# Optimization experiments

Measured on AMD Instinct MI355X. Metric: run time of the kernel, lower is better.

Reference implementation:

```python
import jax, jax.numpy as jnp
import numpy as np
from functools import partial

TAU = 2.0       # membrane time constant
V_TH = 1.0      # firing threshold
SLOPE = 10.0    # surrogate sigmoid slope (matches rate_encode's 10*)
T = 10          # time_window
H = 12          # num_heads


def lif_step(v, I):
    """One LIF update: leaky integrate, surrogate spike, multiplicative reset."""
    v = v + (I - v) / TAU
    spk = jax.nn.sigmoid(SLOPE * (v - V_TH))
    v = v * (1.0 - spk)
    return spk, v


def setup_inputs() -> dict:
    key = jax.random.key(0)
    ks = jax.random.split(key, 5)
    B, S, E = 8, 1024, 768
    scale = 1.0 / np.sqrt(E)
    x = jax.random.uniform(ks[0], (B, S, E), dtype=jnp.float32)
    Wq = jax.random.normal(ks[1], (E, E), dtype=jnp.float32) * scale
    Wk = jax.random.normal(ks[2], (E, E), dtype=jnp.float32) * scale
    Wv = jax.random.normal(ks[3], (E, E), dtype=jnp.float32) * scale
    Wo = jax.random.normal(ks[4], (E, E), dtype=jnp.float32) * scale
    zb = jnp.zeros((E,), dtype=jnp.float32)
    return {"x": x, "Wq": Wq, "bq": zb, "Wk": Wk, "bk": zb,
            "Wv": Wv, "bv": zb, "Wo": Wo, "bo": zb}


def reference(x, Wq, bq, Wk, bk, Wv, bv, Wo, bo):
    B, S, E = x.shape
    D = E // H
    # rate encoding probability (x assumed in [0,1] range, clipped)
    p = jnp.clip(x, 0.0, 1.0)  # [B,S,E]

    def step(carry, t):
        vq, vk, vv, Qa, Ka, Va = carry
        inp = jax.nn.sigmoid(SLOPE * (p * T - t))  # [B,S,E] spikes at step t
        qs, vq = lif_step(vq, inp @ Wq.T + bq)
        ks, vk = lif_step(vk, inp @ Wk.T + bk)
        vs, vv = lif_step(vv, inp @ Wv.T + bv)
        return (vq, vk, vv, Qa + qs, Ka + ks, Va + vs), None

    z = jnp.zeros((B, S, E), dtype=x.dtype)
    t_idx = jnp.arange(T, dtype=x.dtype)
    (vq, vk, vv, Q, K, V), _ = jax.lax.scan(step, (z, z, z, z, z, z), t_idx)

    # split heads: [B,S,E] -> [B,H,S,D]
    Qh = Q.reshape(B, S, H, D)
    Kh = K.reshape(B, S, H, D)
    Vh = V.reshape(B, S, H, D)
    scores = jnp.einsum('bqhd,bkhd->bhqk', Qh, Kh) / np.sqrt(D)
    attn = jax.nn.softmax(scores, axis=-1)
    out_h = jnp.einsum('bhqk,bkhd->bqhd', attn, Vh)  # [B,S,H,D]
    out = out_h.reshape(B, S, E)
    # output LIF projection with fresh (zero) state
    out_spk, _ = lif_step(jnp.zeros_like(out), out @ Wo.T + bo)
    return out_spk
```

## Files before the change

### kernel.cpp

```cpp
#include <hip/hip_runtime.h>
#include <math.h>

constexpr int B_ = 8, S_ = 1024, E_ = 768, H_ = 12, D_ = 64, T_ = 10;
constexpr int N_ = B_ * S_;
constexpr int NE_ = N_ * E_;
constexpr int WE_ = E_ * E_;

typedef __attribute__((ext_vector_type(8))) short bf16x8;
typedef __attribute__((ext_vector_type(4))) float f32x4;

#define MFMA16(a,b,c) __builtin_amdgcn_mfma_f32_16x16x32_bf16(a,b,c,0,0,0)

__device__ __forceinline__ float sigm(float z){ return 1.f/(1.f+__expf(-z)); }
__device__ __forceinline__ unsigned short f2bf(float f){
    unsigned int u = __float_as_uint(f);
    u += 0x7FFFu + ((u>>16)&1u);
    return (unsigned short)(u>>16);
}
__device__ __forceinline__ float bf2f(unsigned short h){
    return __uint_as_float(((unsigned int)h)<<16);
}
__device__ __forceinline__ void gl16(const void* g, void* l){
    __builtin_amdgcn_global_load_lds((const __attribute__((address_space(1))) unsigned int*)g,
                                     (__attribute__((address_space(3))) unsigned int*)l, 16, 0, 0);
}

__global__ __launch_bounds__(256) void encode_k(const float* __restrict__ x,
                                                unsigned short* __restrict__ enc){
    const int i = blockIdx.x*256 + threadIdx.x;
    const float4 a = ((const float4*)x)[2*i];
    const float4 b = ((const float4*)x)[2*i+1];
    float p[8] = {a.x,a.y,a.z,a.w,b.x,b.y,b.z,b.w};
#pragma unroll
    for (int e=0;e<8;++e) p[e] = 100.f*fminf(fmaxf(p[e],0.f),1.f);
#pragma unroll
    for (int t=0;t<T_;++t){
        unsigned int w[4];
#pragma unroll
        for (int e=0;e<4;++e){
            unsigned short u0 = f2bf(sigm(p[2*e]   - 10.f*(float)t));
            unsigned short u1 = f2bf(sigm(p[2*e+1] - 10.f*(float)t));
            w[e] = (unsigned int)u0 | ((unsigned int)u1<<16);
        }
        ((uint4*)(enc + (long)t*NE_))[i] = make_uint4(w[0],w[1],w[2],w[3]);
    }
}

__global__ __launch_bounds__(256) void wsplit_k(const float* __restrict__ Wq, const float* __restrict__ Wk,
        const float* __restrict__ Wv, const float* __restrict__ Wo,
        unsigned short* __restrict__ whi, unsigned short* __restrict__ wlo){
    int gi = blockIdx.x*256 + threadIdx.x;
    int z = gi / (WE_/8);
    int r = gi % (WE_/8);
    const float* W = z==0?Wq : z==1?Wk : z==2?Wv : Wo;
    const float4 a = ((const float4*)W)[2*r];
    const float4 b = ((const float4*)W)[2*r+1];
    float f[8]={a.x,a.y,a.z,a.w,b.x,b.y,b.z,b.w};
    unsigned int h[4], l[4];
#pragma unroll
    for (int e=0;e<4;++e){
        unsigned short h0=f2bf(f[2*e]),   l0=f2bf(f[2*e]  -bf2f(h0));
        unsigned short h1=f2bf(f[2*e+1]), l1=f2bf(f[2*e+1]-bf2f(h1));
        h[e] = (unsigned)h0 | ((unsigned)h1<<16);
        l[e] = (unsigned)l0 | ((unsigned)l1<<16);
    }
    ((uint4*)(whi + (long)z*WE_))[r] = make_uint4(h[0],h[1],h[2],h[3]);
    ((uint4*)(wlo + (long)z*WE_))[r] = make_uint4(l[0],l[1],l[2],l[3]);
}

__global__ __launch_bounds__(256,2) void qkv_k(const unsigned short* __restrict__ enc,
        const unsigned short* __restrict__ whi,
        const float* __restrict__ bq, const float* __restrict__ bk, const float* __restrict__ bv,
        float* __restrict__ Qf, float* __restrict__ Kf, float* __restrict__ Vf){
    const int z = blockIdx.z;
    const unsigned short* Wh = whi + (long)z*WE_;
    const float* bias = z==0?bq : z==1?bk : bv;
    float* Out = z==0?Qf : z==1?Kf : Vf;
    const int row0 = blockIdx.x*128, col0 = blockIdx.y*64;

    __shared__ unsigned short Ab[128*64];
    __shared__ unsigned short Bh[64*64];

    const int tid = threadIdx.x, lane = tid&63, wid = tid>>6;
    const int l15 = lane&15, l4 = lane>>4, l7 = lane&7;
    const int wr = wid>>1, wc = wid&1;

    int aSrc[4], bSrc[2];
#pragma unroll
    for (int s=0;s<4;++s){
        int idx = (wid + s*4)*64 + lane;
        int row = idx>>3, ch = idx&7;
        aSrc[s] = (row0+row)*E_ + ((ch ^ (row&7))<<3);
    }
#pragma unroll
    for (int s=0;s<2;++s){
        int idx = (wid + s*4)*64 + lane;
        int row = idx>>3, ch = idx&7;
        bSrc[s] = (col0+row)*E_ + ((ch ^ (row&7))<<3);
    }

    const int aBase = (wr*64 + l15)*128;
    const int bBase = (wc*32 + l15)*128;
    const int sw[2] = { ((l4^l7)<<4), ((((4+l4))^l7)<<4) };

    f32x4 acc[4][2];
    float vm[4][2][4] = {};
    float qa[4][2][4] = {};
    float bn[2];
#pragma unroll
    for (int n=0;n<2;++n) bn[n] = bias[col0 + wc*32 + n*16 + l15];
    const f32x4 zero4 = {0.f,0.f,0.f,0.f};

    for (int t=0;t<T_;++t){
        const long tb = (long)t*NE_;
#pragma unroll
        for (int m=0;m<4;++m)
#pragma unroll
            for (int n=0;n<2;++n) acc[m][n] = zero4;
        for (int kt=0;kt<12;++kt){
            const int k0 = kt*64;
            __syncthreads();
#pragma unroll
            for (int s=0;s<4;++s)
                gl16(enc + tb + aSrc[s] + k0, &Ab[(wid+s*4)*512]);
#pragma unroll
            for (int s=0;s<2;++s)
                gl16(Wh + bSrc[s] + k0, &Bh[(wid+s*4)*512]);
            __syncthreads();
#pragma unroll
            for (int kk=0;kk<2;++kk){
                bf16x8 af[4], fbh[2];
#pragma unroll
                for (int m=0;m<4;++m)
                    af[m] = *(const bf16x8*)((const char*)Ab + aBase + m*2048 + sw[kk]);
#pragma unroll
                for (int n=0;n<2;++n)
                    fbh[n] = *(const bf16x8*)((const char*)Bh + bBase + n*2048 + sw[kk]);
#pragma unroll
                for (int m=0;m<4;++m)
#pragma unroll
                    for (int n=0;n<2;++n)
                        acc[m][n] = MFMA16(af[m], fbh[n], acc[m][n]);
            }
        }
#pragma unroll
        for (int m=0;m<4;++m)
#pragma unroll
            for (int n=0;n<2;++n)
#pragma unroll
                for (int j=0;j<4;++j){
                    float I = acc[m][n][j] + bn[n];
                    float v = (vm[m][n][j] + I)*0.5f;
                    float s = sigm(10.f*v - 10.f);
                    vm[m][n][j] = v*(1.f - s);
                    qa[m][n][j] += s;
                }
    }
#pragma unroll
    for (int m=0;m<4;++m)
#pragma unroll
        for (int n=0;n<2;++n)
#pragma unroll
            for (int j=0;j<4;++j){
                int row = row0 + wr*64 + m*16 + l4*4 + j;
                int col = col0 + wc*32 + n*16 + l15;
                Out[(long)row*E_ + col] = qa[m][n][j];
            }
}

__global__ __launch_bounds__(256,2) void attn_k2(const float* __restrict__ Qf, const float* __restrict__ Kf,
        const float* __restrict__ Vf, unsigned short* __restrict__ atth, unsigned short* __restrict__ attl){
    const int q0 = blockIdx.x*64;
    const int h  = blockIdx.y;
    const int b  = blockIdx.z;
    const long base = ((long)b*S_)*E_ + h*64;

    __shared__ char smem[65536];
    unsigned short* Qh = (unsigned short*)(smem);
    unsigned short* Ql = (unsigned short*)(smem + 8192);
    unsigned short* Kh = (unsigned short*)(smem + 16384);
    unsigned short* Kl = (unsigned short*)(smem + 24576);
    unsigned short* Vh = (unsigned short*)(smem + 32768);
    unsigned short* Vl = (unsigned short*)(smem + 40960);
    unsigned short* Ph = (unsigned short*)(smem + 49152);
    unsigned short* Pl = (unsigned short*)(smem + 57344);
    float* OT = (float*)(smem + 16384);

    const int tid = threadIdx.x, lane = tid&63, wid = tid>>6;
    const int l15 = lane&15, l4 = lane>>4, l7 = lane&7;
    const int qrow = wid*16 + l15;

    {
        int q = tid>>2, c0 = (tid&3)*2;
        const float* src = Qf + base + (long)(q0+q)*E_ + (tid&3)*16;
        float4 f0=((const float4*)src)[0], f1=((const float4*)src)[1];
        float4 f2=((const float4*)src)[2], f3=((const float4*)src)[3];
        float f[16]={f0.x,f0.y,f0.z,f0.w,f1.x,f1.y,f1.z,f1.w,f2.x,f2.y,f2.z,f2.w,f3.x,f3.y,f3.z,f3.w};
        bf16x8 vh[2], vl[2];
#pragma unroll
        for (int g=0;g<2;++g)
#pragma unroll
            for (int e=0;e<8;++e){
                unsigned short hh = f2bf(f[g*8+e]);
                vh[g][e] = (short)hh;
                vl[g][e] = (short)f2bf(f[g*8+e]-bf2f(hh));
            }
        int by0 = q*128 + (((c0  ) ^ (q&7))<<4);
        int by1 = q*128 + (((c0+1) ^ (q&7))<<4);
        *(bf16x8*)((char*)Qh + by0) = vh[0];
        *(bf16x8*)((char*)Qh + by1) = vh[1];
        *(bf16x8*)((char*)Ql + by0) = vl[0];
        *(bf16x8*)((char*)Ql + by1) = vl[1];
    }
    __syncthreads();
    bf16x8 qfh[2], qfl[2];
#pragma unroll
    for (int kk=0;kk<2;++kk){
        int off = qrow*128 + ((((kk<<2)+l4) ^ l7)<<4);
        qfh[kk] = *(const bf16x8*)((const char*)Qh + off);
        qfl[kk] = *(const bf16x8*)((const char*)Ql + off);
    }

    float mrun = -1e30f, lrun = 0.f;
    f32x4 ot[4];
    const f32x4 zero4 = {0.f,0.f,0.f,0.f};
#pragma unroll
    for (int m=0;m<4;++m) ot[m] = zero4;

    for (int kt=0;kt<16;++kt){
        const int k0 = kt*64;
        __syncthreads();
        {
            int key = tid>>2, c0 = (tid&3)*2;
            const float* src = Kf + base + (long)(k0+key)*E_ + (tid&3)*16;
            float4 f0=((const float4*)src)[0], f1=((const float4*)src)[1];
            float4 f2=((const float4*)src)[2], f3=((const float4*)src)[3];
            float f[16]={f0.x,f0.y,f0.z,f0.w,f1.x,f1.y,f1.z,f1.w,f2.x,f2.y,f2.z,f2.w,f3.x,f3.y,f3.z,f3.w};
            bf16x8 vh[2], vl[2];
#pragma unroll
            for (int g=0;g<2;++g)
#pragma unroll
                for (int e=0;e<8;++e){
                    unsigned short hh = f2bf(f[g*8+e]);
                    vh[g][e] = (short)hh;
                    vl[g][e] = (short)f2bf(f[g*8+e]-bf2f(hh));
                }
            int by0 = key*128 + (((c0  ) ^ (key&7))<<4);
            int by1 = key*128 + (((c0+1) ^ (key&7))<<4);
            *(bf16x8*)((char*)Kh + by0) = vh[0];
            *(bf16x8*)((char*)Kh + by1) = vh[1];
            *(bf16x8*)((char*)Kl + by0) = vl[0];
            *(bf16x8*)((char*)Kl + by1) = vl[1];
        }
#pragma unroll
        for (int rr=0;rr<2;++rr){
            int dq = (tid>>5) + rr*8;
            int kp = tid&31;
            const float* s0 = Vf + base + (long)(k0 + 2*kp)*E_ + dq*4;
            float4 va = *(const float4*)s0;
            float4 vb = *(const float4*)(s0 + E_);
            float fa[4]={va.x,va.y,va.z,va.w}, fb[4]={vb.x,vb.y,vb.z,vb.w};
#pragma unroll
            for (int dd=0;dd<4;++dd){
                int d = dq*4+dd;
                unsigned short ha=f2bf(fa[dd]), hb=f2bf(fb[dd]);
                unsigned short la=f2bf(fa[dd]-bf2f(ha)), lb=f2bf(fb[dd]-bf2f(hb));
                int byte = d*128 + ((kp<<2) ^ ((d&7)<<4));
                *(unsigned int*)((char*)Vh + byte) = (unsigned)ha | ((unsigned)hb<<16);
                *(unsigned int*)((char*)Vl + byte) = (unsigned)la | ((unsigned)lb<<16);
            }
        }
        __syncthreads();
        f32x4 st[4];
#pragma unroll
        for (int m=0;m<4;++m) st[m] = zero4;
#pragma unroll
        for (int kk=0;kk<2;++kk){
            int swo = ((((kk<<2)+l4) ^ l7)<<4);
            bf16x8 kh[4], kl2[4];
#pragma unroll
            for (int m=0;m<4;++m){
                int off = (m*16+l15)*128 + swo;
                kh[m]  = *(const bf16x8*)((const char*)Kh + off);
                kl2[m] = *(const bf16x8*)((const char*)Kl + off);
            }
#pragma unroll
            for (int m=0;m<4;++m){
                st[m] = MFMA16(kh[m],  qfh[kk], st[m]);
                st[m] = MFMA16(kh[m],  qfl[kk], st[m]);
                st[m] = MFMA16(kl2[m], qfh[kk], st[m]);
            }
        }
        float pmax = -1e30f;
#pragma unroll
        for (int m=0;m<4;++m)
#pragma unroll
            for (int j=0;j<4;++j){ st[m][j] *= 0.125f; pmax = fmaxf(pmax, st[m][j]); }
        pmax = fmaxf(pmax, __shfl_xor(pmax,16));
        pmax = fmaxf(pmax, __shfl_xor(pmax,32));
        float mnew = fmaxf(mrun, pmax);
        float alpha = __expf(mrun - mnew);
        float p[16]; float psum = 0.f;
#pragma unroll
        for (int m=0;m<4;++m)
#pragma unroll
            for (int j=0;j<4;++j){ float e = __expf(st[m][j]-mnew); p[m*4+j]=e; psum+=e; }
        psum += __shfl_xor(psum,16);
        psum += __shfl_xor(psum,32);
        lrun = lrun*alpha + psum;
        mrun = mnew;
#pragma unroll
        for (int m=0;m<4;++m)
#pragma unroll
            for (int j=0;j<4;++j) ot[m][j] *= alpha;
#pragma unroll
        for (int m=0;m<4;++m)
#pragma unroll
            for (int jp=0;jp<2;++jp){
                float fx = p[m*4+jp*2], fy = p[m*4+jp*2+1];
                unsigned short hx=f2bf(fx), hy=f2bf(fy);
                unsigned short lx=f2bf(fx-bf2f(hx)), ly=f2bf(fy-bf2f(hy));
                int key = m*16 + l4*4 + jp*2;
                int byte = qrow*128 + ((key<<1) ^ (l7<<4));
                *(unsigned int*)((char*)Ph + byte) = (unsigned)hx | ((unsigned)hy<<16);
                *(unsigned int*)((char*)Pl + byte) = (unsigned)lx | ((unsigned)ly<<16);
            }
#pragma unroll
        for (int kk=0;kk<2;++kk){
            int swo = ((((kk<<2)+l4) ^ l7)<<4);
            bf16x8 pfh = *(const bf16x8*)((const char*)Ph + qrow*128 + swo);
            bf16x8 pfl = *(const bf16x8*)((const char*)Pl + qrow*128 + swo);
#pragma unroll
            for (int m=0;m<4;++m){
                int off = (m*16+l15)*128 + swo;
                bf16x8 vvh = *(const bf16x8*)((const char*)Vh + off);
                bf16x8 vvl = *(const bf16x8*)((const char*)Vl + off);
                ot[m] = MFMA16(vvh, pfh, ot[m]);
                ot[m] = MFMA16(vvh, pfl, ot[m]);
                ot[m] = MFMA16(vvl, pfh, ot[m]);
            }
        }
    }
    __syncthreads();
    float inv = 1.f/lrun;
#pragma unroll
    for (int m=0;m<4;++m)
#pragma unroll
        for (int j=0;j<4;++j){
            int d = m*16 + l4*4 + j;
            OT[qrow*68 + d] = ot[m][j]*inv;
        }
    __syncthreads();
    {
        int q = tid>>2, d0 = (tid&3)*16;
        const float* rp = OT + q*68 + d0;
        float4 f0=((const float4*)rp)[0], f1=((const float4*)rp)[1];
        float4 f2=((const float4*)rp)[2], f3=((const float4*)rp)[3];
        float f[16]={f0.x,f0.y,f0.z,f0.w,f1.x,f1.y,f1.z,f1.w,f2.x,f2.y,f2.z,f2.w,f3.x,f3.y,f3.z,f3.w};
        bf16x8 vh[2], vl[2];
#pragma unroll
        for (int g=0;g<2;++g)
#pragma unroll
            for (int e=0;e<8;++e){
                unsigned short hh = f2bf(f[g*8+e]);
                vh[g][e] = (short)hh;
                vl[g][e] = (short)f2bf(f[g*8+e]-bf2f(hh));
            }
        long o = base + (long)(q0+q)*E_ + d0;
        *(bf16x8*)(atth + o)     = vh[0];
        *(bf16x8*)(atth + o + 8) = vh[1];
        *(bf16x8*)(attl + o)     = vl[0];
        *(bf16x8*)(attl + o + 8) = vl[1];
    }
}

__global__ __launch_bounds__(256,2) void out_k(const unsigned short* __restrict__ Ah_g,
        const unsigned short* __restrict__ Al_g,
        const unsigned short* __restrict__ Wh,
        const float* __restrict__ bias, float* __restrict__ out){
    const int row0 = blockIdx.x*128, col0 = blockIdx.y*64;
    __shared__ unsigned short Ah[128*64], Al[128*64];
    __shared__ unsigned short Bh2[64*64];

    const int tid = threadIdx.x, lane = tid&63, wid = tid>>6;
    const int l15 = lane&15, l4 = lane>>4, l7 = lane&7;
    const int wr = wid>>1, wc = wid&1;

    int aSrc[4], bSrc[2];
#pragma unroll
    for (int s=0;s<4;++s){
        int idx = (wid + s*4)*64 + lane;
        int row = idx>>3, ch = idx&7;
        aSrc[s] = (row0+row)*E_ + ((ch ^ (row&7))<<3);
    }
#pragma unroll
    for (int s=0;s<2;++s){
        int idx = (wid + s*4)*64 + lane;
        int row = idx>>3, ch = idx&7;
        bSrc[s] = (col0+row)*E_ + ((ch ^ (row&7))<<3);
    }
    const int aBase = (wr*64 + l15)*128;
    const int bBase = (wc*32 + l15)*128;
    const int sw[2] = { ((l4^l7)<<4), ((((4+l4))^l7)<<4) };

    f32x4 acc[4][2];
    const f32x4 zero4 = {0.f,0.f,0.f,0.f};
#pragma unroll
    for (int m=0;m<4;++m)
#pragma unroll
        for (int n=0;n<2;++n) acc[m][n] = zero4;

    for (int kt=0;kt<12;++kt){
        const int k0 = kt*64;
        __syncthreads();
#pragma unroll
        for (int s=0;s<4;++s){
            gl16(Ah_g + aSrc[s] + k0, &Ah[(wid+s*4)*512]);
            gl16(Al_g + aSrc[s] + k0, &Al[(wid+s*4)*512]);
        }
#pragma unroll
        for (int s=0;s<2;++s)
            gl16(Wh + bSrc[s] + k0, &Bh2[(wid+s*4)*512]);
        __syncthreads();
#pragma unroll
        for (int kk=0;kk<2;++kk){
            bf16x8 ah[4], al[4], fbh[2];
#pragma unroll
            for (int m=0;m<4;++m){
                ah[m] = *(const bf16x8*)((const char*)Ah + aBase + m*2048 + sw[kk]);
                al[m] = *(const bf16x8*)((const char*)Al + aBase + m*2048 + sw[kk]);
            }
#pragma unroll
            for (int n=0;n<2;++n)
                fbh[n] = *(const bf16x8*)((const char*)Bh2 + bBase + n*2048 + sw[kk]);
#pragma unroll
            for (int m=0;m<4;++m)
#pragma unroll
                for (int n=0;n<2;++n){
                    acc[m][n] = MFMA16(ah[m], fbh[n], acc[m][n]);
                    acc[m][n] = MFMA16(al[m], fbh[n], acc[m][n]);
                }
        }
    }
#pragma unroll
    for (int m=0;m<4;++m)
#pragma unroll
        for (int n=0;n<2;++n){
            float bn = bias[col0 + wc*32 + n*16 + l15];
#pragma unroll
            for (int j=0;j<4;++j){
                int row = row0 + wr*64 + m*16 + l4*4 + j;
                int col = col0 + wc*32 + n*16 + l15;
                float I = acc[m][n][j] + bn;
                out[(long)row*E_ + col] = sigm(5.f*I - 10.f);
            }
        }
}

extern "C" void kernel_launch(void* const* d_in, const int* in_sizes, int n_in,
                              void* d_out, int out_size, void* d_ws, size_t ws_size,
                              hipStream_t stream){
    const float* x  = (const float*)d_in[0];
    const float* Wq = (const float*)d_in[1];
    const float* bq = (const float*)d_in[2];
    const float* Wk = (const float*)d_in[3];
    const float* bk = (const float*)d_in[4];
    const float* Wv = (const float*)d_in[5];
    const float* bv = (const float*)d_in[6];
    const float* Wo = (const float*)d_in[7];
    const float* bo = (const float*)d_in[8];
    float* out = (float*)d_out;

    char* ws = (char*)d_ws;
    unsigned short* enc  = (unsigned short*)ws;
    unsigned short* atth = (unsigned short*)ws;
    unsigned short* attl = (unsigned short*)(ws + (long)NE_*2);
    unsigned short* whi  = (unsigned short*)(ws + 125829120L);
    unsigned short* wlo  = whi + 4L*WE_;
    float* Qf = (float*)(ws + 135266304L);
    float* Kf = Qf + NE_;
    float* Vf = Kf + NE_;

    wsplit_k<<<dim3(4*(WE_/8)/256), 256, 0, stream>>>(Wq,Wk,Wv,Wo,whi,wlo);
    encode_k<<<dim3(NE_/8/256), 256, 0, stream>>>(x,enc);
    qkv_k<<<dim3(64,12,3), 256, 0, stream>>>(enc,whi,bq,bk,bv,Qf,Kf,Vf);
    attn_k2<<<dim3(16,12,8), 256, 0, stream>>>(Qf,Kf,Vf,atth,attl);
    out_k<<<dim3(64,12), 256, 0, stream>>>(atth,attl,whi+3L*WE_,bo,out);
}
```

Baseline: 605.3 us.

## Emit pre-split bf16 Q/K and transposed V from QKV kernel; async-load in attention

Result: slower. 686.0 us (+13.3%).

```diff
diff --git a/kernel.cpp b/kernel.cpp
--- a/kernel.cpp
+++ b/kernel.cpp
@@ -71,11 +71,12 @@
 __global__ __launch_bounds__(256,2) void qkv_k(const unsigned short* __restrict__ enc,
         const unsigned short* __restrict__ whi,
         const float* __restrict__ bq, const float* __restrict__ bk, const float* __restrict__ bv,
-        float* __restrict__ Qf, float* __restrict__ Kf, float* __restrict__ Vf){
+        unsigned short* __restrict__ Qh_g, unsigned short* __restrict__ Ql_g,
+        unsigned short* __restrict__ Kh_g, unsigned short* __restrict__ Kl_g,
+        unsigned short* __restrict__ Vth_g, unsigned short* __restrict__ Vtl_g){
     const int z = blockIdx.z;
     const unsigned short* Wh = whi + (long)z*WE_;
     const float* bias = z==0?bq : z==1?bk : bv;
-    float* Out = z==0?Qf : z==1?Kf : Vf;
     const int row0 = blockIdx.x*128, col0 = blockIdx.y*64;
 
     __shared__ unsigned short Ab[128*64];
@@ -156,32 +157,66 @@
                     qa[m][n][j] += s;
                 }
     }
-#pragma unroll
-    for (int m=0;m<4;++m)
-#pragma unroll
-        for (int n=0;n<2;++n)
-#pragma unroll
-            for (int j=0;j<4;++j){
-                int row = row0 + wr*64 + m*16 + l4*4 + j;
-                int col = col0 + wc*32 + n*16 + l15;
-                Out[(long)row*E_ + col] = qa[m][n][j];
-            }
-}
-
-__global__ __launch_bounds__(256,2) void attn_k2(const float* __restrict__ Qf, const float* __restrict__ Kf,
-        const float* __restrict__ Vf, unsigned short* __restrict__ atth, unsigned short* __restrict__ attl){
+    if (z == 2){
+        const int b = blockIdx.x >> 3;
+        const long vtb = (long)(b*12 + blockIdx.y) * 65536;
+        const int keyb = (blockIdx.x & 7)*128 + wr*64 + l4*4;
+#pragma unroll
+        for (int m=0;m<4;++m)
+#pragma unroll
+            for (int n=0;n<2;++n){
+                const int d = wc*32 + n*16 + l15;
+                unsigned int hw[2], lw[2];
+#pragma unroll
+                for (int jp=0;jp<2;++jp){
+                    float v0 = qa[m][n][jp*2], v1 = qa[m][n][jp*2+1];
+                    unsigned short h0=f2bf(v0), h1=f2bf(v1);
+                    unsigned short l0=f2bf(v0-bf2f(h0)), l1=f2bf(v1-bf2f(h1));
+                    hw[jp] = (unsigned)h0 | ((unsigned)h1<<16);
+                    lw[jp] = (unsigned)l0 | ((unsigned)l1<<16);
+                }
+                long o = vtb + (long)d*1024 + keyb + m*16;
+                *(uint2*)&Vth_g[o] = make_uint2(hw[0],hw[1]);
+                *(uint2*)&Vtl_g[o] = make_uint2(lw[0],lw[1]);
+            }
+    } else {
+        unsigned short* Oh = (z==0) ? Qh_g : Kh_g;
+        unsigned short* Ol = (z==0) ? Ql_g : Kl_g;
+#pragma unroll
+        for (int m=0;m<4;++m)
+#pragma unroll
+            for (int n=0;n<2;++n)
+#pragma unroll
+                for (int j=0;j<4;++j){
+                    int row = row0 + wr*64 + m*16 + l4*4 + j;
+                    int col = col0 + wc*32 + n*16 + l15;
+                    float v = qa[m][n][j];
+                    unsigned short hh = f2bf(v);
+                    unsigned short ll = f2bf(v - bf2f(hh));
+                    Oh[(long)row*E_ + col] = hh;
+                    Ol[(long)row*E_ + col] = ll;
+                }
+    }
+}
+
+__global__ __launch_bounds__(256,2) void attn_k2(
+        const unsigned short* __restrict__ Qh_g, const unsigned short* __restrict__ Ql_g,
+        const unsigned short* __restrict__ Kh_g, const unsigned short* __restrict__ Kl_g,
+        const unsigned short* __restrict__ Vth_g, const unsigned short* __restrict__ Vtl_g,
+        unsigned short* __restrict__ atth, unsigned short* __restrict__ attl){
     const int q0 = blockIdx.x*64;
     const int h  = blockIdx.y;
     const int b  = blockIdx.z;
     const long base = ((long)b*S_)*E_ + h*64;
+    const long vtb  = (long)(b*12 + h) * 65536;
 
     __shared__ char smem[65536];
-    unsigned short* Qh = (unsigned short*)(smem);
-    unsigned short* Ql = (unsigned short*)(smem + 8192);
-    unsigned short* Kh = (unsigned short*)(smem + 16384);
-    unsigned short* Kl = (unsigned short*)(smem + 24576);
-    unsigned short* Vh = (unsigned short*)(smem + 32768);
-    unsigned short* Vl = (unsigned short*)(smem + 40960);
+    unsigned short* QhL = (unsigned short*)(smem);
+    unsigned short* QlL = (unsigned short*)(smem + 8192);
+    unsigned short* KhL = (unsigned short*)(smem + 16384);
+    unsigned short* KlL = (unsigned short*)(smem + 24576);
+    unsigned short* VhL = (unsigned short*)(smem + 32768);
+    unsigned short* VlL = (unsigned short*)(smem + 40960);
     unsigned short* Ph = (unsigned short*)(smem + 49152);
     unsigned short* Pl = (unsigned short*)(smem + 57344);
     float* OT = (float*)(smem + 16384);
@@ -190,35 +225,27 @@
     const int l15 = lane&15, l4 = lane>>4, l7 = lane&7;
     const int qrow = wid*16 + l15;
 
-    {
-        int q = tid>>2, c0 = (tid&3)*2;
-        const float* src = Qf + base + (long)(q0+q)*E_ + (tid&3)*16;
-        float4 f0=((const float4*)src)[0], f1=((const float4*)src)[1];
-        float4 f2=((const float4*)src)[2], f3=((const float4*)src)[3];
-        float f[16]={f0.x,f0.y,f0.z,f0.w,f1.x,f1.y,f1.z,f1.w,f2.x,f2.y,f2.z,f2.w,f3.x,f3.y,f3.z,f3.w};
-        bf16x8 vh[2], vl[2];
-#pragma unroll
-        for (int g=0;g<2;++g)
-#pragma unroll
-            for (int e=0;e<8;++e){
-                unsigned short hh = f2bf(f[g*8+e]);
-                vh[g][e] = (short)hh;
-                vl[g][e] = (short)f2bf(f[g*8+e]-bf2f(hh));
-            }
-        int by0 = q*128 + (((c0  ) ^ (q&7))<<4);
-        int by1 = q*128 + (((c0+1) ^ (q&7))<<4);
-        *(bf16x8*)((char*)Qh + by0) = vh[0];
-        *(bf16x8*)((char*)Qh + by1) = vh[1];
-        *(bf16x8*)((char*)Ql + by0) = vl[0];
-        *(bf16x8*)((char*)Ql + by1) = vl[1];
+    int sOff[2], vOff[2];
+#pragma unroll
+    for (int s=0;s<2;++s){
+        int idx = (wid + s*4)*64 + lane;
+        int r = idx>>3, c = idx&7;
+        sOff[s] = r*E_ + ((c ^ (r&7))<<3);
+        vOff[s] = (r<<10) + ((c ^ (r&7))<<3);
+    }
+
+#pragma unroll
+    for (int s=0;s<2;++s){
+        gl16(Qh_g + base + (long)q0*E_ + sOff[s], &QhL[(wid+s*4)*512]);
+        gl16(Ql_g + base + (long)q0*E_ + sOff[s], &QlL[(wid+s*4)*512]);
     }
     __syncthreads();
     bf16x8 qfh[2], qfl[2];
 #pragma unroll
     for (int kk=0;kk<2;++kk){
         int off = qrow*128 + ((((kk<<2)+l4) ^ l7)<<4);
-        qfh[kk] = *(const bf16x8*)((const char*)Qh + off);
-        qfl[kk] = *(const bf16x8*)((const char*)Ql + off);
+        qfh[kk] = *(const bf16x8*)((const char*)QhL + off);
+        qfl[kk] = *(const bf16x8*)((const char*)QlL + off);
     }
 
     float mrun = -1e30f, lrun = 0.f;
@@ -230,45 +257,12 @@
     for (int kt=0;kt<16;++kt){
         const int k0 = kt*64;
         __syncthreads();
-        {
-            int key = tid>>2, c0 = (tid&3)*2;
-            const float* src = Kf + base + (long)(k0+key)*E_ + (tid&3)*16;
-            float4 f0=((const float4*)src)[0], f1=((const float4*)src)[1];
-            float4 f2=((const float4*)src)[2], f3=((const float4*)src)[3];
-            float f[16]={f0.x,f0.y,f0.z,f0.w,f1.x,f1.y,f1.z,f1.w,f2.x,f2.y,f2.z,f2.w,f3.x,f3.y,f3.z,f3.w};
-            bf16x8 vh[2], vl[2];
-#pragma unroll
-            for (int g=0;g<2;++g)
-#pragma unroll
-                for (int e=0;e<8;++e){
-                    unsigned short hh = f2bf(f[g*8+e]);
-                    vh[g][e] = (short)hh;
-                    vl[g][e] = (short)f2bf(f[g*8+e]-bf2f(hh));
-                }
-            int by0 = key*128 + (((c0  ) ^ (key&7))<<4);
-            int by1 = key*128 + (((c0+1) ^ (key&7))<<4);
-            *(bf16x8*)((char*)Kh + by0) = vh[0];
-            *(bf16x8*)((char*)Kh + by1) = vh[1];
-            *(bf16x8*)((char*)Kl + by0) = vl[0];
-            *(bf16x8*)((char*)Kl + by1) = vl[1];
-        }
-#pragma unroll
-        for (int rr=0;rr<2;++rr){
-            int dq = (tid>>5) + rr*8;
-            int kp = tid&31;
-            const float* s0 = Vf + base + (long)(k0 + 2*kp)*E_ + dq*4;
-            float4 va = *(const float4*)s0;
-            float4 vb = *(const float4*)(s0 + E_);
-            float fa[4]={va.x,va.y,va.z,va.w}, fb[4]={vb.x,vb.y,vb.z,vb.w};
-#pragma unroll
-            for (int dd=0;dd<4;++dd){
-                int d = dq*4+dd;
-                unsigned short ha=f2bf(fa[dd]), hb=f2bf(fb[dd]);
-                unsigned short la=f2bf(fa[dd]-bf2f(ha)), lb=f2bf(fb[dd]-bf2f(hb));
-                int byte = d*128 + ((kp<<2) ^ ((d&7)<<4));
-                *(unsigned int*)((char*)Vh + byte) = (unsigned)ha | ((unsigned)hb<<16);
-                *(unsigned int*)((char*)Vl + byte) = (unsigned)la | ((unsigned)lb<<16);
-            }
+#pragma unroll
+        for (int s=0;s<2;++s){
+            gl16(Kh_g + base + (long)k0*E_ + sOff[s], &KhL[(wid+s*4)*512]);
+            gl16(Kl_g + base + (long)k0*E_ + sOff[s], &KlL[(wid+s*4)*512]);
+            gl16(Vth_g + vtb + k0 + vOff[s], &VhL[(wid+s*4)*512]);
+            gl16(Vtl_g + vtb + k0 + vOff[s], &VlL[(wid+s*4)*512]);
         }
         __syncthreads();
         f32x4 st[4];
@@ -281,8 +275,8 @@
 #pragma unroll
             for (int m=0;m<4;++m){
                 int off = (m*16+l15)*128 + swo;
-                kh[m]  = *(const bf16x8*)((const char*)Kh + off);
-                kl2[m] = *(const bf16x8*)((const char*)Kl + off);
+                kh[m]  = *(const bf16x8*)((const char*)KhL + off);
+                kl2[m] = *(const bf16x8*)((const char*)KlL + off);
             }
 #pragma unroll
             for (int m=0;m<4;++m){
@@ -333,8 +327,8 @@
 #pragma unroll
             for (int m=0;m<4;++m){
                 int off = (m*16+l15)*128 + swo;
-                bf16x8 vvh = *(const bf16x8*)((const char*)Vh + off);
-                bf16x8 vvl = *(const bf16x8*)((const char*)Vl + off);
+                bf16x8 vvh = *(const bf16x8*)((const char*)VhL + off);
+                bf16x8 vvl = *(const bf16x8*)((const char*)VlL + off);
                 ot[m] = MFMA16(vvh, pfh, ot[m]);
                 ot[m] = MFMA16(vvh, pfl, ot[m]);
                 ot[m] = MFMA16(vvl, pfh, ot[m]);
@@ -477,13 +471,18 @@
     unsigned short* attl = (unsigned short*)(ws + (long)NE_*2);
     unsigned short* whi  = (unsigned short*)(ws + 125829120L);
     unsigned short* wlo  = whi + 4L*WE_;
-    float* Qf = (float*)(ws + 135266304L);
-    float* Kf = Qf + NE_;
-    float* Vf = Kf + NE_;
+    unsigned short* Qh_g  = (unsigned short*)(ws + 135266304L);
+    unsigned short* Ql_g  = Qh_g + NE_;
+    unsigned short* Kh_g  = Ql_g + NE_;
+    unsigned short* Kl_g  = Kh_g + NE_;
+    unsigned short* Vth_g = Kl_g + NE_;
+    unsigned short* Vtl_g = Vth_g + NE_;
 
     wsplit_k<<<dim3(4*(WE_/8)/256), 256, 0, stream>>>(Wq,Wk,Wv,Wo,whi,wlo);
     encode_k<<<dim3(NE_/8/256), 256, 0, stream>>>(x,enc);
-    qkv_k<<<dim3(64,12,3), 256, 0, stream>>>(enc,whi,bq,bk,bv,Qf,Kf,Vf);
-    attn_k2<<<dim3(16,12,8), 256, 0, stream>>>(Qf,Kf,Vf,atth,attl);
+    qkv_k<<<dim3(64,12,3), 256, 0, stream>>>(enc,whi,bq,bk,bv,
+                                             Qh_g,Ql_g,Kh_g,Kl_g,Vth_g,Vtl_g);
+    attn_k2<<<dim3(16,12,8), 256, 0, stream>>>(Qh_g,Ql_g,Kh_g,Kl_g,Vth_g,Vtl_g,
+                                               atth,attl);
     out_k<<<dim3(64,12), 256, 0, stream>>>(atth,attl,whi+3L*WE_,bo,out);
 }
```
